# Kernel optimization log

Measured on AMD Instinct MI355X. Metric: run time of the kernel, lower is better.

Reference implementation:

```python
import jax, jax.numpy as jnp
import numpy as np

B, T, H, W, C = 8, 16, 64, 64, 16
HID = 64  # hidden_dim of each ConvLSTM cell
K = 3     # kernel size


def _convlstm_step(x, h, c, Wk, b):
    # conv over concat([x, h]) -> 4*HID gate channels (i, f, o, g)
    z = jax.lax.conv_general_dilated(
        jnp.concatenate([x, h], axis=-1), Wk,
        window_strides=(1, 1), padding='SAME',
        dimension_numbers=('NHWC', 'HWIO', 'NHWC')) + b
    i, f, o, g = jnp.split(z, 4, axis=-1)
    c_new = jax.nn.sigmoid(f) * c + jax.nn.sigmoid(i) * jnp.tanh(g)
    h_new = jax.nn.sigmoid(o) * jnp.tanh(c_new)
    return h_new, c_new


def setup_inputs() -> dict:
    key = jax.random.key(0)
    k1, k2, k3 = jax.random.split(key, 3)
    enc_input = jax.random.normal(k1, (B, T, H, W, C), jnp.float32)
    # input cell: in_channels = C + HID; stacked hidden cell: 2*HID
    W0 = jax.random.normal(k2, (K, K, C + HID, 4 * HID), jnp.float32) * 0.05
    b0 = jnp.zeros((4 * HID,), jnp.float32)
    W1 = jax.random.normal(k3, (K, K, 2 * HID, 4 * HID), jnp.float32) * 0.05
    b1 = jnp.zeros((4 * HID,), jnp.float32)
    return {"enc_input": enc_input, "W0": W0, "b0": b0, "W1": W1, "b1": b1}


def reference(enc_input, W0, b0, W1, b1):
    Bv, Tv, Hv, Wv, _ = enc_input.shape
    z0 = jnp.zeros((Bv, Hv, Wv, HID), enc_input.dtype)

    def step(carry, x_t):
        h0, c0, h1, c1 = carry
        h0, c0 = _convlstm_step(x_t, h0, c0, W0, b0)   # input ConvLSTM
        h1, c1 = _convlstm_step(h0, h1, c1, W1, b1)    # stacked hidden ConvLSTM
        return (h0, c0, h1, c1), None

    xs = jnp.moveaxis(enc_input, 1, 0)  # [T, B, H, W, C]
    (h0, c0, h1, c1), _ = jax.lax.scan(step, (z0, z0, z0, z0), xs)
    # Encoder returns last hidden layer's (h, c)
    return (h1, c1)
```

## Files before the change

### kernel.cpp

```cpp
#include <hip/hip_runtime.h>
#include <hip/hip_bf16.h>

#define Bv 8
#define Tv 16
#define Hv 64
#define Wv 64
#define Cv 16
#define HID 64
#define PH 66

typedef short short8 __attribute__((ext_vector_type(8)));
typedef float f32x4 __attribute__((ext_vector_type(4)));
typedef unsigned short u16x8 __attribute__((ext_vector_type(8)));

__device__ __forceinline__ unsigned short f2bf(float x) {
  union { float f; unsigned int u; } v; v.f = x;
  unsigned int r = v.u + 0x7FFF + ((v.u >> 16) & 1);
  return (unsigned short)(r >> 16);
}
__device__ __forceinline__ float sigmoid_f(float x) {
  return 1.f / (1.f + __expf(-x));
}
__device__ __forceinline__ float tanh_f(float x) {
  float e = __expf(2.f * x);
  return 1.f - 2.f / (e + 1.f);
}
__device__ __forceinline__ void waitv(int n) {
  if      (n <= 0) asm volatile("s_waitcnt vmcnt(0)" ::: "memory");
  else if (n == 5) asm volatile("s_waitcnt vmcnt(5)" ::: "memory");
  else             asm volatile("s_waitcnt vmcnt(10)" ::: "memory");
}

__global__ void relayout_w0(const float* __restrict__ W0, unsigned short* __restrict__ out) {
  int o = blockIdx.x * 256 + threadIdx.x;
  if (o >= 27 * 8192) return;
  int cc = o >> 13, t = o & 8191;
  int wn = t >> 11, t2 = t & 2047;
  int g = t2 >> 9, t3 = t2 & 511;
  int l = t3 >> 3, e = t3 & 7;
  int kg = l >> 4, r = l & 15;
  int k = kg * 8 + e;
  int col = g * 64 + wn * 16 + r;
  int tap = cc / 3, cgi = cc - tap * 3;
  int p = cgi * 32 + k;
  float v = 0.f;
  if (p < 16)        v = W0[(size_t)(tap * 80 + p) * 256 + col];
  else if (p >= 32)  v = W0[(size_t)(tap * 80 + (p - 16)) * 256 + col];
  out[o] = f2bf(v);
}
__global__ void relayout_w1(const float* __restrict__ W1, unsigned short* __restrict__ out) {
  int o = blockIdx.x * 256 + threadIdx.x;
  if (o >= 36 * 8192) return;
  int cc = o >> 13, t = o & 8191;
  int wn = t >> 11, t2 = t & 2047;
  int g = t2 >> 9, t3 = t2 & 511;
  int l = t3 >> 3, e = t3 & 7;
  int kg = l >> 4, r = l & 15;
  int k = kg * 8 + e;
  int col = g * 64 + wn * 16 + r;
  int tap = cc >> 2, cgi = cc & 3;
  out[o] = f2bf(W1[(size_t)(tap * 128 + cgi * 32 + k) * 256 + col]);
}

__global__ void zero_init(unsigned short* __restrict__ h0a, unsigned short* __restrict__ h0b,
                          unsigned short* __restrict__ h1a, unsigned short* __restrict__ h1b,
                          unsigned short* __restrict__ xb) {
  int idx = blockIdx.x * 256 + threadIdx.x;
  u16x8 z = {};
  const int XB_CH = (Bv * PH * PH * 32 * 2 * 2) / 16;
  if (idx < XB_CH) { *(u16x8*)(xb + idx * 8) = z; return; }
  idx -= XB_CH;
  int bufi = idx / 16640;
  if (bufi >= 4) return;
  int rem = idx - bufi * 16640;
  int b = rem / 2080, r2 = rem - b * 2080;
  int hp = r2 >> 3, c8 = r2 & 7;
  int y, x;
  if (hp < 66)       { y = 0;  x = hp; }
  else if (hp < 132) { y = 65; x = hp - 66; }
  else { int i2 = hp - 132; y = 1 + (i2 >> 1); x = (i2 & 1) * 65; }
  unsigned short* base = (bufi == 0) ? h0a : (bufi == 1) ? h0b : (bufi == 2) ? h1a : h1b;
  *(u16x8*)(base + ((size_t)((b * PH + y) * PH) + x) * 64 + c8 * 8) = z;
}

__global__ void convert_x0(const float* __restrict__ enc, unsigned short* __restrict__ xb) {
  int idx = blockIdx.x * 256 + threadIdx.x;
  int b = idx >> 12, pix = idx & 4095;
  int y = pix >> 6, x = pix & 63;
  const float* s = enc + ((size_t)(b * Tv + 0) * 4096 + pix) * 16;
  float4 f0 = *(const float4*)(s);
  float4 f1 = *(const float4*)(s + 4);
  float4 f2 = *(const float4*)(s + 8);
  float4 f3 = *(const float4*)(s + 12);
  u16x8 o0, o1;
  o0[0]=f2bf(f0.x); o0[1]=f2bf(f0.y); o0[2]=f2bf(f0.z); o0[3]=f2bf(f0.w);
  o0[4]=f2bf(f1.x); o0[5]=f2bf(f1.y); o0[6]=f2bf(f1.z); o0[7]=f2bf(f1.w);
  o1[0]=f2bf(f2.x); o1[1]=f2bf(f2.y); o1[2]=f2bf(f2.z); o1[3]=f2bf(f2.w);
  o1[4]=f2bf(f3.x); o1[5]=f2bf(f3.y); o1[6]=f2bf(f3.z); o1[7]=f2bf(f3.w);
  unsigned short* d = xb + ((size_t)((b * PH + y + 1) * PH) + (x + 1)) * 32;
  *(u16x8*)(d)     = o0;
  *(u16x8*)(d + 8) = o1;
}

template<int CELL, int NC>
__device__ __forceinline__ void cell_run(
    const char* __restrict__ A0, const char* __restrict__ A1,
    const char* __restrict__ Wr, const float* __restrict__ bias,
    float* __restrict__ cbuf, unsigned short* __restrict__ hout,
    float* __restrict__ h1fin, float* __restrict__ c1fin,
    char* lds, int b, int by, int bx, int tid)
{
  constexpr bool T0C = (CELL == 0) ? (NC == 9) : (NC == 18);
  const int l = tid & 63, w = tid >> 6;
  const int r = l & 15, kg = l >> 4;
  const int j = w * 16 + r;

  int pixs;
  {
    int ps = w * 16 + r;
    int ys = by * 8 + (ps >> 3), xs = bx * 8 + (ps & 7);
    pixs = (b * PH + ys) * PH + xs;
  }

  float bi[4];
#pragma unroll
  for (int g = 0; g < 4; ++g) bi[g] = bias[g * 64 + j];
  float cpre[4][4] = {};
  if constexpr (!T0C) {
#pragma unroll
    for (int mi = 0; mi < 4; ++mi) {
#pragma unroll
      for (int rg = 0; rg < 4; ++rg) {
        int p = mi * 16 + kg * 4 + rg;
        int y = by * 8 + (p >> 3), x = bx * 8 + (p & 7);
        cpre[mi][rg] = cbuf[((size_t)((b * Hv + y) * Wv) + x) * HID + j];
      }
    }
  }

  auto ISSUE = [&](int cc, int buf) {
    char* dst = lds + buf * 20480;
    int tap, cgi, wcc;
    if (CELL == 0) {
      if (T0C) { tap = cc; cgi = 0; wcc = cc * 3; }
      else     { tap = cc / 3; cgi = cc - tap * 3; wcc = cc; }
    } else {
      if (T0C) { tap = cc >> 1; cgi = cc & 1; wcc = tap * 4 + cgi; }
      else     { tap = cc >> 2; cgi = cc & 3; wcc = cc; }
    }
    int ky = tap / 3, kx = tap - ky * 3;
    const char* srcb;
    unsigned aoff;
    if (CELL == 0) {
      if (cgi == 0) { srcb = A0; aoff = (unsigned)((pixs + ky * PH + kx) * 64 + kg * 16); }
      else { srcb = A1;
             aoff = (unsigned)((pixs + ky * PH + kx) * 128 + ((cgi == 2) ? 64 : 0) + kg * 16); }
    } else {
      srcb = (cgi < 2) ? A0 : A1;
      aoff = (unsigned)((pixs + ky * PH + kx) * 128 + (cgi & 1) * 64 + kg * 16);
    }
    __builtin_amdgcn_global_load_lds((const unsigned int*)(srcb + aoff),
                                     (unsigned int*)(dst + w * 1024), 16, 0, 0);
    const char* wp = Wr + (size_t)wcc * 16384 + (unsigned)(w * 4096 + l * 16);
#pragma unroll
    for (int k = 0; k < 4; ++k)
      __builtin_amdgcn_global_load_lds((const unsigned int*)(wp + k * 1024),
                                       (unsigned int*)(dst + 4096 + w * 4096 + k * 1024), 16, 0, 0);
  };

  f32x4 acc[4][4] = {};
  short8 af[2][4], bfv[2][4];

  ISSUE(0, 0); ISSUE(1, 1);
#pragma unroll
  for (int cc = 0; cc < NC; ++cc) {
    waitv(cc <= NC - 2 ? 5 : 0);
    __builtin_amdgcn_sched_barrier(0);
    __builtin_amdgcn_s_barrier();
    __builtin_amdgcn_sched_barrier(0);

    const int q = cc & 1;
    const char* bufp = lds + (cc % 3) * 20480;
#pragma unroll
    for (int mi = 0; mi < 4; ++mi)
      af[q][mi] = *(const short8*)(bufp + mi * 1024 + l * 16);
#pragma unroll
    for (int g = 0; g < 4; ++g)
      bfv[q][g] = *(const short8*)(bufp + 4096 + w * 4096 + g * 1024 + l * 16);

    if (cc > 0) {
      asm volatile("s_waitcnt lgkmcnt(8)" ::: "memory");
      __builtin_amdgcn_sched_barrier(0);
    }
    if (cc + 2 < NC) ISSUE(cc + 2, (cc + 2) % 3);
    __builtin_amdgcn_sched_barrier(0);

    if (cc > 0) {
      const int qp = q ^ 1;
#pragma unroll
      for (int mi = 0; mi < 4; ++mi)
#pragma unroll
        for (int g = 0; g < 4; ++g)
          acc[mi][g] = __builtin_amdgcn_mfma_f32_16x16x32_bf16(
              af[qp][mi], bfv[qp][g], acc[mi][g], 0, 0, 0);
    }
  }
  asm volatile("s_waitcnt lgkmcnt(0)" ::: "memory");
  __builtin_amdgcn_sched_barrier(0);
  {
    const int qp = (NC - 1) & 1;
#pragma unroll
    for (int mi = 0; mi < 4; ++mi)
#pragma unroll
      for (int g = 0; g < 4; ++g)
        acc[mi][g] = __builtin_amdgcn_mfma_f32_16x16x32_bf16(
            af[qp][mi], bfv[qp][g], acc[mi][g], 0, 0, 0);
  }

#pragma unroll
  for (int mi = 0; mi < 4; ++mi) {
#pragma unroll
    for (int rg = 0; rg < 4; ++rg) {
      int p = mi * 16 + kg * 4 + rg;
      int y = by * 8 + (p >> 3), x = bx * 8 + (p & 7);
      float zi = acc[mi][0][rg] + bi[0];
      float zf = acc[mi][1][rg] + bi[1];
      float zo = acc[mi][2][rg] + bi[2];
      float zg = acc[mi][3][rg] + bi[3];
      float co = cpre[mi][rg];
      float cn = sigmoid_f(zf) * co + sigmoid_f(zi) * tanh_f(zg);
      float hn = sigmoid_f(zo) * tanh_f(cn);
      size_t ci = ((size_t)((b * Hv + y) * Wv) + x) * HID + j;
      cbuf[ci] = cn;
      hout[((size_t)((b * PH + y + 1) * PH) + (x + 1)) * HID + j] = f2bf(hn);
      if (CELL == 1 && h1fin != nullptr) {
        h1fin[ci] = hn;
        c1fin[ci] = cn;
      }
    }
  }
}

template<int NC1, int NC0, bool LAST>
__global__ __launch_bounds__(256, 2)
void step_fused(const unsigned short* __restrict__ xbr, unsigned short* __restrict__ xbw,
                const unsigned short* __restrict__ h0r, unsigned short* __restrict__ h0w,
                const unsigned short* __restrict__ h1r, unsigned short* __restrict__ h1w,
                const unsigned short* __restrict__ w0r, const unsigned short* __restrict__ w1r,
                const float* __restrict__ b0, const float* __restrict__ b1,
                float* __restrict__ c0, float* __restrict__ c1,
                float* __restrict__ h1f, float* __restrict__ c1f,
                const float* __restrict__ enc, int tnext)
{
  extern __shared__ char lds[];
  const int tid = threadIdx.x;
  const int gid = blockIdx.x;
  int isC1, tile;
  if constexpr (NC1 > 0 && NC0 > 0) { isC1 = gid & 1; tile = gid >> 1; }
  else if constexpr (NC1 > 0)       { isC1 = 1; tile = gid; }
  else                              { isC1 = 0; tile = gid; }
  const int b = tile >> 6, rem = tile & 63;
  const int by = rem >> 3, bx = rem & 7;

  if constexpr (NC1 > 0) {
    if (isC1) {
      cell_run<1, NC1>((const char*)h0r, (const char*)h1r, (const char*)w1r, b1,
                       c1, h1w, LAST ? h1f : nullptr, LAST ? c1f : nullptr,
                       lds, b, by, bx, tid);
      return;
    }
  }
  if constexpr (NC0 > 0) {
    cell_run<0, NC0>((const char*)xbr, (const char*)h0r, (const char*)w0r, b0,
                     c0, h0w, nullptr, nullptr, lds, b, by, bx, tid);
    if (tnext >= 0) {
      int pp = tid >> 2, q4 = tid & 3;
      int y = by * 8 + (pp >> 3), x = bx * 8 + (pp & 7);
      const float* s = enc + ((size_t)(b * Tv + tnext) * 4096 + (y * 64 + x)) * 16 + q4 * 4;
      float4 f = *(const float4*)s;
      unsigned short* d = xbw + ((size_t)((b * PH + y + 1) * PH) + (x + 1)) * 32 + q4 * 4;
      d[0] = f2bf(f.x); d[1] = f2bf(f.y); d[2] = f2bf(f.z); d[3] = f2bf(f.w);
    }
  }
}

extern "C" void kernel_launch(void* const* d_in, const int* in_sizes, int n_in,
                              void* d_out, int out_size, void* d_ws, size_t ws_size,
                              hipStream_t stream) {
  const float* enc = (const float*)d_in[0];
  const float* W0  = (const float*)d_in[1];
  const float* b0  = (const float*)d_in[2];
  const float* W1  = (const float*)d_in[3];
  const float* b1  = (const float*)d_in[4];

  float* out = (float*)d_out;
  const size_t NST = (size_t)Bv * Hv * Wv * HID;
  float* h1f = out;
  float* c1  = out + NST;

  char* ws = (char*)d_ws;
  const size_t SZ_C = NST * 4;
  const size_t SZ_H = (size_t)Bv * PH * PH * HID * 2;
  const size_t SZ_X = (size_t)Bv * PH * PH * 32 * 2;
  float*          c0  = (float*)ws;
  unsigned short* h0a = (unsigned short*)(ws + SZ_C);
  unsigned short* h0b = (unsigned short*)(ws + SZ_C + SZ_H);
  unsigned short* h1a = (unsigned short*)(ws + SZ_C + 2 * SZ_H);
  unsigned short* h1b = (unsigned short*)(ws + SZ_C + 3 * SZ_H);
  unsigned short* xb0 = (unsigned short*)(ws + SZ_C + 4 * SZ_H);
  unsigned short* xb1 = (unsigned short*)(ws + SZ_C + 4 * SZ_H + SZ_X);
  unsigned short* w0r = (unsigned short*)(ws + SZ_C + 4 * SZ_H + 2 * SZ_X);
  unsigned short* w1r = (unsigned short*)(ws + SZ_C + 4 * SZ_H + 2 * SZ_X + (size_t)27 * 16384);

  hipFuncSetAttribute((const void*)step_fused<0,9,false>,  hipFuncAttributeMaxDynamicSharedMemorySize, 65536);
  hipFuncSetAttribute((const void*)step_fused<18,27,false>,hipFuncAttributeMaxDynamicSharedMemorySize, 65536);
  hipFuncSetAttribute((const void*)step_fused<36,27,false>,hipFuncAttributeMaxDynamicSharedMemorySize, 65536);
  hipFuncSetAttribute((const void*)step_fused<36,0,true>,  hipFuncAttributeMaxDynamicSharedMemorySize, 65536);

  zero_init<<<1349, 256, 0, stream>>>(h0a, h0b, h1a, h1b, xb0);
  relayout_w0<<<864, 256, 0, stream>>>(W0, w0r);
  relayout_w1<<<1152, 256, 0, stream>>>(W1, w1r);
  convert_x0<<<128, 256, 0, stream>>>(enc, xb0);

  const int LDSB = 61440;
  step_fused<0,9,false><<<512, 256, LDSB, stream>>>(
      xb0, xb1, h0b, h0a, h1a, h1b, w0r, w1r, b0, b1, c0, c1,
      nullptr, nullptr, enc, 1);
  for (int t = 1; t <= 15; ++t) {
    unsigned short* h0r = (t & 1) ? h0a : h0b;
    unsigned short* h0w = (t & 1) ? h0b : h0a;
    unsigned short* h1r = (t & 1) ? h1b : h1a;
    unsigned short* h1w = (t & 1) ? h1a : h1b;
    unsigned short* xr  = (t & 1) ? xb1 : xb0;
    unsigned short* xw  = (t & 1) ? xb0 : xb1;
    int tn = (t + 1 <= 15) ? (t + 1) : -1;
    if (t == 1)
      step_fused<18,27,false><<<1024, 256, LDSB, stream>>>(
          xr, xw, h0r, h0w, h1r, h1w, w0r, w1r, b0, b1, c0, c1,
          nullptr, nullptr, enc, tn);
    else
      step_fused<36,27,false><<<1024, 256, LDSB, stream>>>(
          xr, xw, h0r, h0w, h1r, h1w, w0r, w1r, b0, b1, c0, c1,
          nullptr, nullptr, enc, tn);
  }
  step_fused<36,0,true><<<512, 256, LDSB, stream>>>(
      xb0, xb1, h0b, h0a, h1a, h1b, w0r, w1r, b0, b1, c0, c1,
      h1f, c1, enc, -1);
}
```

Baseline: 746.6 us.

## Retile ConvLSTM step blocks to 128 pixels × 128 gate columns

Each block now covers a 16x8 pixel tile and half of the gate columns (selected by gh), with waves arranged 2x2 over pixels and columns, instead of 64 pixels by all 256 columns. This cuts the per-chunk LDS stage from 20 KB to 16 KB, so the triple buffer fits in 48 KB and launch bounds rise to 3 blocks per CU for higher occupancy. Block indexing is reordered with the batch index innermost, and the next-frame input conversion is done only by gh==0 blocks, with 8 channels per thread. The cost is that activation tiles are loaded twice, once per column half, and the weight tile per block is halved.

```diff
diff --git a/kernel.cpp b/kernel.cpp
--- a/kernel.cpp
+++ b/kernel.cpp
@@ -26,9 +26,8 @@
   return 1.f - 2.f / (e + 1.f);
 }
 __device__ __forceinline__ void waitv(int n) {
-  if      (n <= 0) asm volatile("s_waitcnt vmcnt(0)" ::: "memory");
-  else if (n == 5) asm volatile("s_waitcnt vmcnt(5)" ::: "memory");
-  else             asm volatile("s_waitcnt vmcnt(10)" ::: "memory");
+  if (n <= 0) asm volatile("s_waitcnt vmcnt(0)" ::: "memory");
+  else        asm volatile("s_waitcnt vmcnt(4)" ::: "memory");
 }
 
 __global__ void relayout_w0(const float* __restrict__ W0, unsigned short* __restrict__ out) {
@@ -108,18 +107,21 @@
     const char* __restrict__ Wr, const float* __restrict__ bias,
     float* __restrict__ cbuf, unsigned short* __restrict__ hout,
     float* __restrict__ h1fin, float* __restrict__ c1fin,
-    char* lds, int b, int by, int bx, int tid)
+    char* lds, int b, int by, int bx, int gh, int tid)
 {
   constexpr bool T0C = (CELL == 0) ? (NC == 9) : (NC == 18);
   const int l = tid & 63, w = tid >> 6;
+  const int wm = w >> 1, wn2 = w & 1;
+  const int wn = gh * 2 + wn2;
   const int r = l & 15, kg = l >> 4;
-  const int j = w * 16 + r;
-
-  int pixs;
-  {
-    int ps = w * 16 + r;
-    int ys = by * 8 + (ps >> 3), xs = bx * 8 + (ps & 7);
-    pixs = (b * PH + ys) * PH + xs;
+  const int j = wn * 16 + r;
+
+  int pixs[2];
+#pragma unroll
+  for (int i = 0; i < 2; ++i) {
+    int ps = (2 * w + i) * 16 + r;
+    int ys = by * 16 + (ps >> 3), xs = bx * 8 + (ps & 7);
+    pixs[i] = (b * PH + ys) * PH + xs;
   }
 
   float bi[4];
@@ -131,15 +133,15 @@
     for (int mi = 0; mi < 4; ++mi) {
 #pragma unroll
       for (int rg = 0; rg < 4; ++rg) {
-        int p = mi * 16 + kg * 4 + rg;
-        int y = by * 8 + (p >> 3), x = bx * 8 + (p & 7);
+        int p = wm * 64 + mi * 16 + kg * 4 + rg;
+        int y = by * 16 + (p >> 3), x = bx * 8 + (p & 7);
         cpre[mi][rg] = cbuf[((size_t)((b * Hv + y) * Wv) + x) * HID + j];
       }
     }
   }
 
   auto ISSUE = [&](int cc, int buf) {
-    char* dst = lds + buf * 20480;
+    char* dst = lds + buf * 16384;
     int tap, cgi, wcc;
     if (CELL == 0) {
       if (T0C) { tap = cc; cgi = 0; wcc = cc * 3; }
@@ -150,22 +152,25 @@
     }
     int ky = tap / 3, kx = tap - ky * 3;
     const char* srcb;
-    unsigned aoff;
+    int chb, cho;
     if (CELL == 0) {
-      if (cgi == 0) { srcb = A0; aoff = (unsigned)((pixs + ky * PH + kx) * 64 + kg * 16); }
-      else { srcb = A1;
-             aoff = (unsigned)((pixs + ky * PH + kx) * 128 + ((cgi == 2) ? 64 : 0) + kg * 16); }
+      if (cgi == 0) { srcb = A0; chb = 64; cho = 0; }
+      else          { srcb = A1; chb = 128; cho = (cgi == 2) ? 64 : 0; }
     } else {
       srcb = (cgi < 2) ? A0 : A1;
-      aoff = (unsigned)((pixs + ky * PH + kx) * 128 + (cgi & 1) * 64 + kg * 16);
-    }
-    __builtin_amdgcn_global_load_lds((const unsigned int*)(srcb + aoff),
-                                     (unsigned int*)(dst + w * 1024), 16, 0, 0);
-    const char* wp = Wr + (size_t)wcc * 16384 + (unsigned)(w * 4096 + l * 16);
-#pragma unroll
-    for (int k = 0; k < 4; ++k)
-      __builtin_amdgcn_global_load_lds((const unsigned int*)(wp + k * 1024),
-                                       (unsigned int*)(dst + 4096 + w * 4096 + k * 1024), 16, 0, 0);
+      chb = 128; cho = (cgi & 1) * 64;
+    }
+#pragma unroll
+    for (int i = 0; i < 2; ++i) {
+      unsigned aoff = (unsigned)((pixs[i] + ky * PH + kx) * chb + cho + kg * 16);
+      __builtin_amdgcn_global_load_lds((const unsigned int*)(srcb + aoff),
+                                       (unsigned int*)(dst + (2 * w + i) * 1024), 16, 0, 0);
+    }
+    const char* wp = Wr + (size_t)wcc * 16384 + (unsigned)(gh * 8192 + w * 2048 + l * 16);
+    __builtin_amdgcn_global_load_lds((const unsigned int*)(wp),
+                                     (unsigned int*)(dst + 8192 + w * 2048), 16, 0, 0);
+    __builtin_amdgcn_global_load_lds((const unsigned int*)(wp + 1024),
+                                     (unsigned int*)(dst + 8192 + w * 2048 + 1024), 16, 0, 0);
   };
 
   f32x4 acc[4][4] = {};
@@ -174,19 +179,19 @@
   ISSUE(0, 0); ISSUE(1, 1);
 #pragma unroll
   for (int cc = 0; cc < NC; ++cc) {
-    waitv(cc <= NC - 2 ? 5 : 0);
+    waitv(cc <= NC - 2 ? 4 : 0);
     __builtin_amdgcn_sched_barrier(0);
     __builtin_amdgcn_s_barrier();
     __builtin_amdgcn_sched_barrier(0);
 
     const int q = cc & 1;
-    const char* bufp = lds + (cc % 3) * 20480;
+    const char* bufp = lds + (cc % 3) * 16384;
 #pragma unroll
     for (int mi = 0; mi < 4; ++mi)
-      af[q][mi] = *(const short8*)(bufp + mi * 1024 + l * 16);
+      af[q][mi] = *(const short8*)(bufp + (wm * 4 + mi) * 1024 + l * 16);
 #pragma unroll
     for (int g = 0; g < 4; ++g)
-      bfv[q][g] = *(const short8*)(bufp + 4096 + w * 4096 + g * 1024 + l * 16);
+      bfv[q][g] = *(const short8*)(bufp + 8192 + wn2 * 4096 + g * 1024 + l * 16);
 
     if (cc > 0) {
       asm volatile("s_waitcnt lgkmcnt(8)" ::: "memory");
@@ -221,8 +226,8 @@
   for (int mi = 0; mi < 4; ++mi) {
 #pragma unroll
     for (int rg = 0; rg < 4; ++rg) {
-      int p = mi * 16 + kg * 4 + rg;
-      int y = by * 8 + (p >> 3), x = bx * 8 + (p & 7);
+      int p = wm * 64 + mi * 16 + kg * 4 + rg;
+      int y = by * 16 + (p >> 3), x = bx * 8 + (p & 7);
       float zi = acc[mi][0][rg] + bi[0];
       float zf = acc[mi][1][rg] + bi[1];
       float zo = acc[mi][2][rg] + bi[2];
@@ -242,7 +247,7 @@
 }
 
 template<int NC1, int NC0, bool LAST>
-__global__ __launch_bounds__(256, 2)
+__global__ __launch_bounds__(256, 3)
 void step_fused(const unsigned short* __restrict__ xbr, unsigned short* __restrict__ xbw,
                 const unsigned short* __restrict__ h0r, unsigned short* __restrict__ h0w,
                 const unsigned short* __restrict__ h1r, unsigned short* __restrict__ h1w,
@@ -255,31 +260,35 @@
   extern __shared__ char lds[];
   const int tid = threadIdx.x;
   const int gid = blockIdx.x;
-  int isC1, tile;
-  if constexpr (NC1 > 0 && NC0 > 0) { isC1 = gid & 1; tile = gid >> 1; }
-  else if constexpr (NC1 > 0)       { isC1 = 1; tile = gid; }
-  else                              { isC1 = 0; tile = gid; }
-  const int b = tile >> 6, rem = tile & 63;
-  const int by = rem >> 3, bx = rem & 7;
+  const int b = gid & 7;
+  int k = gid >> 3;
+  int isC1;
+  if constexpr (NC1 > 0 && NC0 > 0) { isC1 = k & 1; k >>= 1; }
+  else if constexpr (NC1 > 0)       { isC1 = 1; }
+  else                              { isC1 = 0; }
+  const int gh = k & 1, tile = k >> 1;
+  const int by = tile >> 3, bx = tile & 7;
 
   if constexpr (NC1 > 0) {
     if (isC1) {
       cell_run<1, NC1>((const char*)h0r, (const char*)h1r, (const char*)w1r, b1,
                        c1, h1w, LAST ? h1f : nullptr, LAST ? c1f : nullptr,
-                       lds, b, by, bx, tid);
+                       lds, b, by, bx, gh, tid);
       return;
     }
   }
   if constexpr (NC0 > 0) {
     cell_run<0, NC0>((const char*)xbr, (const char*)h0r, (const char*)w0r, b0,
-                     c0, h0w, nullptr, nullptr, lds, b, by, bx, tid);
-    if (tnext >= 0) {
-      int pp = tid >> 2, q4 = tid & 3;
-      int y = by * 8 + (pp >> 3), x = bx * 8 + (pp & 7);
-      const float* s = enc + ((size_t)(b * Tv + tnext) * 4096 + (y * 64 + x)) * 16 + q4 * 4;
-      float4 f = *(const float4*)s;
-      unsigned short* d = xbw + ((size_t)((b * PH + y + 1) * PH) + (x + 1)) * 32 + q4 * 4;
-      d[0] = f2bf(f.x); d[1] = f2bf(f.y); d[2] = f2bf(f.z); d[3] = f2bf(f.w);
+                     c0, h0w, nullptr, nullptr, lds, b, by, bx, gh, tid);
+    if (tnext >= 0 && gh == 0) {
+      int pp = tid >> 1, q8 = tid & 1;
+      int y = by * 16 + (pp >> 3), x = bx * 8 + (pp & 7);
+      const float* s = enc + ((size_t)(b * Tv + tnext) * 4096 + (y * 64 + x)) * 16 + q8 * 8;
+      float4 f0 = *(const float4*)s;
+      float4 f1 = *(const float4*)(s + 4);
+      unsigned short* d = xbw + ((size_t)((b * PH + y + 1) * PH) + (x + 1)) * 32 + q8 * 8;
+      d[0] = f2bf(f0.x); d[1] = f2bf(f0.y); d[2] = f2bf(f0.z); d[3] = f2bf(f0.w);
+      d[4] = f2bf(f1.x); d[5] = f2bf(f1.y); d[6] = f2bf(f1.z); d[7] = f2bf(f1.w);
     }
   }
 }
@@ -312,17 +321,12 @@
   unsigned short* w0r = (unsigned short*)(ws + SZ_C + 4 * SZ_H + 2 * SZ_X);
   unsigned short* w1r = (unsigned short*)(ws + SZ_C + 4 * SZ_H + 2 * SZ_X + (size_t)27 * 16384);
 
-  hipFuncSetAttribute((const void*)step_fused<0,9,false>,  hipFuncAttributeMaxDynamicSharedMemorySize, 65536);
-  hipFuncSetAttribute((const void*)step_fused<18,27,false>,hipFuncAttributeMaxDynamicSharedMemorySize, 65536);
-  hipFuncSetAttribute((const void*)step_fused<36,27,false>,hipFuncAttributeMaxDynamicSharedMemorySize, 65536);
-  hipFuncSetAttribute((const void*)step_fused<36,0,true>,  hipFuncAttributeMaxDynamicSharedMemorySize, 65536);
-
   zero_init<<<1349, 256, 0, stream>>>(h0a, h0b, h1a, h1b, xb0);
   relayout_w0<<<864, 256, 0, stream>>>(W0, w0r);
   relayout_w1<<<1152, 256, 0, stream>>>(W1, w1r);
   convert_x0<<<128, 256, 0, stream>>>(enc, xb0);
 
-  const int LDSB = 61440;
+  const int LDSB = 49152;
   step_fused<0,9,false><<<512, 256, LDSB, stream>>>(
       xb0, xb1, h0b, h0a, h1a, h1b, w0r, w1r, b0, b1, c0, c1,
       nullptr, nullptr, enc, 1);
```

Result: slower. 927.2 us (+24.2%).

## Enlarge tile to 128 pixels with 8 waves in a 2x4 grid

Applied to the files above, without the earlier changes.

Each block now covers a 16x8 pixel tile using 512 threads arranged as 2 M-waves by 4 N-waves. This halves the number of weight-tile loads per output pixel, and each wave loads only part of the weight tile. The register double-buffering of MFMA fragments is removed: the kernel now waits for all LDS reads (lgkmcnt 0) before issuing MFMAs, and the c-state preload moves to after the main loop. The larger LDS footprint and block size may reduce occupancy, and the simpler pipeline exposes more LDS latency.

```diff
diff --git a/kernel.cpp b/kernel.cpp
--- a/kernel.cpp
+++ b/kernel.cpp
@@ -24,11 +24,6 @@
 __device__ __forceinline__ float tanh_f(float x) {
   float e = __expf(2.f * x);
   return 1.f - 2.f / (e + 1.f);
-}
-__device__ __forceinline__ void waitv(int n) {
-  if      (n <= 0) asm volatile("s_waitcnt vmcnt(0)" ::: "memory");
-  else if (n == 5) asm volatile("s_waitcnt vmcnt(5)" ::: "memory");
-  else             asm volatile("s_waitcnt vmcnt(10)" ::: "memory");
 }
 
 __global__ void relayout_w0(const float* __restrict__ W0, unsigned short* __restrict__ out) {
@@ -112,34 +107,19 @@
 {
   constexpr bool T0C = (CELL == 0) ? (NC == 9) : (NC == 18);
   const int l = tid & 63, w = tid >> 6;
+  const int wm = w >> 2, wn = w & 3;
   const int r = l & 15, kg = l >> 4;
-  const int j = w * 16 + r;
+  const int j = wn * 16 + r;
 
   int pixs;
   {
     int ps = w * 16 + r;
-    int ys = by * 8 + (ps >> 3), xs = bx * 8 + (ps & 7);
+    int ys = by * 16 + (ps >> 3), xs = bx * 8 + (ps & 7);
     pixs = (b * PH + ys) * PH + xs;
   }
 
-  float bi[4];
-#pragma unroll
-  for (int g = 0; g < 4; ++g) bi[g] = bias[g * 64 + j];
-  float cpre[4][4] = {};
-  if constexpr (!T0C) {
-#pragma unroll
-    for (int mi = 0; mi < 4; ++mi) {
-#pragma unroll
-      for (int rg = 0; rg < 4; ++rg) {
-        int p = mi * 16 + kg * 4 + rg;
-        int y = by * 8 + (p >> 3), x = bx * 8 + (p & 7);
-        cpre[mi][rg] = cbuf[((size_t)((b * Hv + y) * Wv) + x) * HID + j];
-      }
-    }
-  }
-
   auto ISSUE = [&](int cc, int buf) {
-    char* dst = lds + buf * 20480;
+    char* dst = lds + buf * 24576;
     int tap, cgi, wcc;
     if (CELL == 0) {
       if (T0C) { tap = cc; cgi = 0; wcc = cc * 3; }
@@ -161,74 +141,73 @@
     }
     __builtin_amdgcn_global_load_lds((const unsigned int*)(srcb + aoff),
                                      (unsigned int*)(dst + w * 1024), 16, 0, 0);
-    const char* wp = Wr + (size_t)wcc * 16384 + (unsigned)(w * 4096 + l * 16);
-#pragma unroll
-    for (int k = 0; k < 4; ++k)
-      __builtin_amdgcn_global_load_lds((const unsigned int*)(wp + k * 1024),
-                                       (unsigned int*)(dst + 4096 + w * 4096 + k * 1024), 16, 0, 0);
+    const char* wp = Wr + (size_t)wcc * 16384 + (unsigned)(w * 2048 + l * 16);
+    __builtin_amdgcn_global_load_lds((const unsigned int*)(wp),
+                                     (unsigned int*)(dst + 8192 + w * 2048), 16, 0, 0);
+    __builtin_amdgcn_global_load_lds((const unsigned int*)(wp + 1024),
+                                     (unsigned int*)(dst + 8192 + w * 2048 + 1024), 16, 0, 0);
   };
 
   f32x4 acc[4][4] = {};
-  short8 af[2][4], bfv[2][4];
+  short8 af[4], bfv[4];
 
   ISSUE(0, 0); ISSUE(1, 1);
 #pragma unroll
   for (int cc = 0; cc < NC; ++cc) {
-    waitv(cc <= NC - 2 ? 5 : 0);
+    if (cc <= NC - 2) { asm volatile("s_waitcnt vmcnt(3)" ::: "memory"); }
+    else              { asm volatile("s_waitcnt vmcnt(0)" ::: "memory"); }
     __builtin_amdgcn_sched_barrier(0);
     __builtin_amdgcn_s_barrier();
     __builtin_amdgcn_sched_barrier(0);
 
-    const int q = cc & 1;
-    const char* bufp = lds + (cc % 3) * 20480;
+    const char* bufp = lds + (cc % 3) * 24576;
 #pragma unroll
     for (int mi = 0; mi < 4; ++mi)
-      af[q][mi] = *(const short8*)(bufp + mi * 1024 + l * 16);
+      af[mi] = *(const short8*)(bufp + (wm * 4 + mi) * 1024 + l * 16);
 #pragma unroll
     for (int g = 0; g < 4; ++g)
-      bfv[q][g] = *(const short8*)(bufp + 4096 + w * 4096 + g * 1024 + l * 16);
-
-    if (cc > 0) {
-      asm volatile("s_waitcnt lgkmcnt(8)" ::: "memory");
-      __builtin_amdgcn_sched_barrier(0);
-    }
+      bfv[g] = *(const short8*)(bufp + 8192 + (wn * 4 + g) * 1024 + l * 16);
+
+    asm volatile("s_waitcnt lgkmcnt(0)" ::: "memory");
+    __builtin_amdgcn_sched_barrier(0);
     if (cc + 2 < NC) ISSUE(cc + 2, (cc + 2) % 3);
     __builtin_amdgcn_sched_barrier(0);
 
-    if (cc > 0) {
-      const int qp = q ^ 1;
-#pragma unroll
-      for (int mi = 0; mi < 4; ++mi)
-#pragma unroll
-        for (int g = 0; g < 4; ++g)
-          acc[mi][g] = __builtin_amdgcn_mfma_f32_16x16x32_bf16(
-              af[qp][mi], bfv[qp][g], acc[mi][g], 0, 0, 0);
-    }
-  }
-  asm volatile("s_waitcnt lgkmcnt(0)" ::: "memory");
-  __builtin_amdgcn_sched_barrier(0);
-  {
-    const int qp = (NC - 1) & 1;
 #pragma unroll
     for (int mi = 0; mi < 4; ++mi)
 #pragma unroll
       for (int g = 0; g < 4; ++g)
         acc[mi][g] = __builtin_amdgcn_mfma_f32_16x16x32_bf16(
-            af[qp][mi], bfv[qp][g], acc[mi][g], 0, 0, 0);
-  }
-
+            af[mi], bfv[g], acc[mi][g], 0, 0, 0);
+  }
+
+  float bi[4];
+#pragma unroll
+  for (int g = 0; g < 4; ++g) bi[g] = bias[g * 64 + j];
+  float cpre[4][4];
 #pragma unroll
   for (int mi = 0; mi < 4; ++mi) {
 #pragma unroll
     for (int rg = 0; rg < 4; ++rg) {
-      int p = mi * 16 + kg * 4 + rg;
-      int y = by * 8 + (p >> 3), x = bx * 8 + (p & 7);
+      if constexpr (T0C) { cpre[mi][rg] = 0.f; }
+      else {
+        int p = wm * 64 + mi * 16 + kg * 4 + rg;
+        int y = by * 16 + (p >> 3), x = bx * 8 + (p & 7);
+        cpre[mi][rg] = cbuf[((size_t)((b * Hv + y) * Wv) + x) * HID + j];
+      }
+    }
+  }
+#pragma unroll
+  for (int mi = 0; mi < 4; ++mi) {
+#pragma unroll
+    for (int rg = 0; rg < 4; ++rg) {
+      int p = wm * 64 + mi * 16 + kg * 4 + rg;
+      int y = by * 16 + (p >> 3), x = bx * 8 + (p & 7);
       float zi = acc[mi][0][rg] + bi[0];
       float zf = acc[mi][1][rg] + bi[1];
       float zo = acc[mi][2][rg] + bi[2];
       float zg = acc[mi][3][rg] + bi[3];
-      float co = cpre[mi][rg];
-      float cn = sigmoid_f(zf) * co + sigmoid_f(zi) * tanh_f(zg);
+      float cn = sigmoid_f(zf) * cpre[mi][rg] + sigmoid_f(zi) * tanh_f(zg);
       float hn = sigmoid_f(zo) * tanh_f(cn);
       size_t ci = ((size_t)((b * Hv + y) * Wv) + x) * HID + j;
       cbuf[ci] = cn;
@@ -242,7 +221,7 @@
 }
 
 template<int NC1, int NC0, bool LAST>
-__global__ __launch_bounds__(256, 2)
+__global__ __launch_bounds__(512, 4)
 void step_fused(const unsigned short* __restrict__ xbr, unsigned short* __restrict__ xbw,
                 const unsigned short* __restrict__ h0r, unsigned short* __restrict__ h0w,
                 const unsigned short* __restrict__ h1r, unsigned short* __restrict__ h1w,
@@ -255,11 +234,11 @@
   extern __shared__ char lds[];
   const int tid = threadIdx.x;
   const int gid = blockIdx.x;
-  int isC1, tile;
-  if constexpr (NC1 > 0 && NC0 > 0) { isC1 = gid & 1; tile = gid >> 1; }
-  else if constexpr (NC1 > 0)       { isC1 = 1; tile = gid; }
-  else                              { isC1 = 0; tile = gid; }
-  const int b = tile >> 6, rem = tile & 63;
+  int isC1, k;
+  if constexpr (NC1 > 0 && NC0 > 0) { isC1 = gid & 1; k = gid >> 1; }
+  else if constexpr (NC1 > 0)       { isC1 = 1; k = gid; }
+  else                              { isC1 = 0; k = gid; }
+  const int b = k >> 5, rem = k & 31;
   const int by = rem >> 3, bx = rem & 7;
 
   if constexpr (NC1 > 0) {
@@ -275,7 +254,7 @@
                      c0, h0w, nullptr, nullptr, lds, b, by, bx, tid);
     if (tnext >= 0) {
       int pp = tid >> 2, q4 = tid & 3;
-      int y = by * 8 + (pp >> 3), x = bx * 8 + (pp & 7);
+      int y = by * 16 + (pp >> 3), x = bx * 8 + (pp & 7);
       const float* s = enc + ((size_t)(b * Tv + tnext) * 4096 + (y * 64 + x)) * 16 + q4 * 4;
       float4 f = *(const float4*)s;
       unsigned short* d = xbw + ((size_t)((b * PH + y + 1) * PH) + (x + 1)) * 32 + q4 * 4;
@@ -312,18 +291,18 @@
   unsigned short* w0r = (unsigned short*)(ws + SZ_C + 4 * SZ_H + 2 * SZ_X);
   unsigned short* w1r = (unsigned short*)(ws + SZ_C + 4 * SZ_H + 2 * SZ_X + (size_t)27 * 16384);
 
-  hipFuncSetAttribute((const void*)step_fused<0,9,false>,  hipFuncAttributeMaxDynamicSharedMemorySize, 65536);
-  hipFuncSetAttribute((const void*)step_fused<18,27,false>,hipFuncAttributeMaxDynamicSharedMemorySize, 65536);
-  hipFuncSetAttribute((const void*)step_fused<36,27,false>,hipFuncAttributeMaxDynamicSharedMemorySize, 65536);
-  hipFuncSetAttribute((const void*)step_fused<36,0,true>,  hipFuncAttributeMaxDynamicSharedMemorySize, 65536);
+  hipFuncSetAttribute((const void*)step_fused<0,9,false>,   hipFuncAttributeMaxDynamicSharedMemorySize, 73728);
+  hipFuncSetAttribute((const void*)step_fused<18,27,false>, hipFuncAttributeMaxDynamicSharedMemorySize, 73728);
+  hipFuncSetAttribute((const void*)step_fused<36,27,false>, hipFuncAttributeMaxDynamicSharedMemorySize, 73728);
+  hipFuncSetAttribute((const void*)step_fused<36,0,true>,   hipFuncAttributeMaxDynamicSharedMemorySize, 73728);
 
   zero_init<<<1349, 256, 0, stream>>>(h0a, h0b, h1a, h1b, xb0);
   relayout_w0<<<864, 256, 0, stream>>>(W0, w0r);
   relayout_w1<<<1152, 256, 0, stream>>>(W1, w1r);
   convert_x0<<<128, 256, 0, stream>>>(enc, xb0);
 
-  const int LDSB = 61440;
-  step_fused<0,9,false><<<512, 256, LDSB, stream>>>(
+  const int LDSB = 73728;
+  step_fused<0,9,false><<<256, 512, LDSB, stream>>>(
       xb0, xb1, h0b, h0a, h1a, h1b, w0r, w1r, b0, b1, c0, c1,
       nullptr, nullptr, enc, 1);
   for (int t = 1; t <= 15; ++t) {
@@ -335,15 +314,15 @@
     unsigned short* xw  = (t & 1) ? xb0 : xb1;
     int tn = (t + 1 <= 15) ? (t + 1) : -1;
     if (t == 1)
-      step_fused<18,27,false><<<1024, 256, LDSB, stream>>>(
+      step_fused<18,27,false><<<512, 512, LDSB, stream>>>(
           xr, xw, h0r, h0w, h1r, h1w, w0r, w1r, b0, b1, c0, c1,
           nullptr, nullptr, enc, tn);
     else
-      step_fused<36,27,false><<<1024, 256, LDSB, stream>>>(
+      step_fused<36,27,false><<<512, 512, LDSB, stream>>>(
           xr, xw, h0r, h0w, h1r, h1w, w0r, w1r, b0, b1, c0, c1,
           nullptr, nullptr, enc, tn);
   }
-  step_fused<36,0,true><<<512, 256, LDSB, stream>>>(
+  step_fused<36,0,true><<<256, 512, LDSB, stream>>>(
       xb0, xb1, h0b, h0a, h1a, h1b, w0r, w1r, b0, b1, c0, c1,
       h1f, c1, enc, -1);
 }
```

Measured after the change: 671.8 us. -10.0%, faster.
